# Optimization experiments

Hardware: AMD Instinct MI355X
Metric: run time of the kernel (lower is better)

## Reference

```python
import jax, jax.numpy as jnp
import numpy as np

N_NODES = 100000
IN_FEATS = 256
N_EDGES = 3200000
N_SEL = 4096
J_POOL = 50  # eval branch: inner loop over first 50 selected nodes


def setup_inputs() -> dict:
    key = jax.random.key(0)
    ks = jax.random.split(key, 16)
    x = jax.random.normal(ks[0], (N_NODES, IN_FEATS), dtype=jnp.float32)
    edge_index = jax.random.randint(ks[1], (2, N_EDGES), 0, N_NODES)
    nodes = jax.random.randint(ks[2], (N_SEL,), 0, N_NODES)
    s1 = 1.0 / np.sqrt(IN_FEATS)
    s2 = 1.0 / np.sqrt(32)
    s3 = 1.0 / np.sqrt(16)
    return {
        "x": x,
        "w1": jax.random.uniform(ks[3], (IN_FEATS, 32), jnp.float32, -s1, s1),
        "b1": jnp.zeros((32,), jnp.float32),
        "w2": jax.random.uniform(ks[4], (32, 16), jnp.float32, -s2, s2),
        "b2": jnp.zeros((16,), jnp.float32),
        "gate1_w": jax.random.normal(ks[5], (32, 4), jnp.float32) * 0.02,
        "e1_w": jax.random.uniform(ks[6], (4, 32, 16), jnp.float32, -s2, s2),
        "e1_b": jnp.zeros((4, 16), jnp.float32),
        "gate2_w": jax.random.normal(ks[7], (16, 4), jnp.float32) * 0.02,
        "e2_w": jax.random.uniform(ks[8], (4, 16, 2), jnp.float32, -s3, s3),
        "e2_b": jnp.zeros((4, 2), jnp.float32),
        "edge_index": edge_index,
        "nodes": nodes,
    }


def _gcn_conv(h, w, b, src, dst, n):
    hw = h @ w
    deg = jnp.zeros((n,), hw.dtype).at[dst].add(1.0)
    dis = jax.lax.rsqrt(jnp.maximum(deg, 1e-12))
    norm = dis[src] * dis[dst]
    msg = hw[src] * norm[:, None]
    return jax.ops.segment_sum(msg, dst, num_segments=n) + b


def _moe_top1(z, gate_w, ew, eb):
    # k=1 gating: softmax over a single selected logit == weight 1.0
    idx = jnp.argmax(z @ gate_w, axis=-1)              # [M]
    outs = jnp.einsum('mi,eio->meo', z, ew) + eb        # [M, E, O]
    return jnp.take_along_axis(outs, idx[:, None, None], axis=1)[:, 0]


def reference(x, w1, b1, w2, b2, gate1_w, e1_w, e1_b, gate2_w, e2_w, e2_b,
              edge_index, nodes):
    n = x.shape[0]
    loops = jnp.arange(n)
    src = jnp.concatenate([edge_index[0], loops])
    dst = jnp.concatenate([edge_index[1], loops])

    h = jax.nn.relu(_gcn_conv(x, w1, b1, src, dst, n))   # dropout: eval mode (identity)
    h = _gcn_conv(h, w2, b2, src, dst, n)                # [N, 16]

    # eval branch pairwise concat: i over all selected nodes, j over first 50
    hi = jnp.repeat(h[nodes], J_POOL, axis=0)            # [M, 16]
    hj = jnp.tile(h[nodes[:J_POOL]], (nodes.shape[0], 1))  # [M, 16]
    x_sim = jnp.concatenate([hi, hj], axis=-1)           # [M, 32]

    z = jax.nn.relu(_moe_top1(x_sim, gate1_w, e1_w, e1_b))
    z = _moe_top1(z, gate2_w, e2_w, e2_b)                # [M, 2]
    return jax.nn.log_softmax(z, axis=1), x_sim
```

## Files before the change

kernel.cpp:

```cpp
#include <hip/hip_runtime.h>
#include <hip/hip_fp16.h>
#include <math.h>


#define NPB 64
#define NB_PAD 2048
#define BATCH 8192
#define NSCAP 12288

typedef _Float16 half8 __attribute__((ext_vector_type(8)));
typedef float f32x4 __attribute__((ext_vector_type(4)));

__global__ void zero_kernel(int* __restrict__ p, int c) {
    int i = blockIdx.x * 256 + threadIdx.x;
    if (i < c) p[i] = 0;
}

__global__ __launch_bounds__(256) void histA_kernel(const int* __restrict__ ei,
                                                    int* __restrict__ bhist, int nE, int nb) {
    __shared__ int h[NB_PAD];
    int tid = threadIdx.x;
    for (int t = tid; t < nb; t += 256) h[t] = 0;
    __syncthreads();
    int base = blockIdx.x * 4096;
    for (int t = tid; t < 4096; t += 256) {
        int e = base + t;
        if (e < nE) atomicAdd(&h[ei[nE + e] >> 6], 1);
    }
    __syncthreads();
    for (int t = tid; t < nb; t += 256) { int c = h[t]; if (c) atomicAdd(&bhist[t], c); }
}

__global__ __launch_bounds__(256) void scanB_kernel(const int* __restrict__ bhist,
                                                    int* __restrict__ boffs,
                                                    int* __restrict__ gcur, int nb) {
    int t = threadIdx.x;
    int v[8], s = 0;
    #pragma unroll
    for (int i = 0; i < 8; ++i) { int c = t * 8 + i; v[i] = (c < nb) ? bhist[c] : 0; s += v[i]; }
    int lane = t & 63, wid = t >> 6;
    int incl = s;
    for (int d = 1; d < 64; d <<= 1) { int u = __shfl_up(incl, (unsigned)d, 64); if (lane >= d) incl += u; }
    __shared__ int ws[4];
    if (lane == 63) ws[wid] = incl;
    __syncthreads();
    int add = 0;
    for (int w = 0; w < wid; ++w) add += ws[w];
    incl += add;
    int excl = incl - s;
    #pragma unroll
    for (int i = 0; i < 8; ++i) {
        int c = t * 8 + i;
        if (c < nb) { boffs[c] = excl; gcur[c] = excl; }
        excl += v[i];
    }
    if (t == 0) boffs[nb] = ws[0] + ws[1] + ws[2] + ws[3];
}

__global__ __launch_bounds__(256) void scatterC_kernel(const int* __restrict__ ei,
                                                       int* __restrict__ gcur,
                                                       int* __restrict__ keys, int nE, int nb) {
    __shared__ int kbuf[BATCH];
    __shared__ unsigned short kbk[BATCH];
    __shared__ int lstart[NB_PAD];
    __shared__ int cursor[NB_PAD];
    __shared__ int gbase[NB_PAD];
    __shared__ int ws2[4];
    int tid = threadIdx.x;
    int base = blockIdx.x * BATCH;
    int cnt = nE - base; if (cnt > BATCH) cnt = BATCH;
    for (int t = tid; t < nb; t += 256) lstart[t] = 0;
    __syncthreads();
    for (int t = tid; t < cnt; t += 256)
        atomicAdd(&lstart[ei[nE + base + t] >> 6], 1);
    __syncthreads();
    {
        int v[8], s = 0;
        #pragma unroll
        for (int i = 0; i < 8; ++i) { int c = tid * 8 + i; v[i] = (c < nb) ? lstart[c] : 0; s += v[i]; }
        int lane = tid & 63, wid = tid >> 6;
        int incl = s;
        for (int d = 1; d < 64; d <<= 1) { int u = __shfl_up(incl, (unsigned)d, 64); if (lane >= d) incl += u; }
        if (lane == 63) ws2[wid] = incl;
        __syncthreads();
        int add = 0;
        for (int w = 0; w < wid; ++w) add += ws2[w];
        incl += add;
        int excl = incl - s;
        #pragma unroll
        for (int i = 0; i < 8; ++i) {
            int c = tid * 8 + i;
            if (c < nb) { lstart[c] = excl; cursor[c] = excl; }
            excl += v[i];
        }
    }
    __syncthreads();
    for (int t = tid; t < nb; t += 256) {
        int e = (t == nb - 1) ? cnt : lstart[t + 1];
        int c = e - lstart[t];
        gbase[t] = c ? atomicAdd(&gcur[t], c) : 0;
    }
    for (int t = tid; t < cnt; t += 256) {
        int d = ei[nE + base + t];
        int s = ei[base + t];
        int b = d >> 6;
        int pos = atomicAdd(&cursor[b], 1);
        kbuf[pos] = s | ((d & 63) << 17);
        kbk[pos] = (unsigned short)b;
    }
    __syncthreads();
    for (int j = tid; j < cnt; j += 256) {
        int b = kbk[j];
        keys[gbase[b] + (j - lstart[b])] = kbuf[j];
    }
}

__global__ __launch_bounds__(256) void nodesort_kernel(int* __restrict__ keys,
                                                       const int* __restrict__ boffs,
                                                       int* __restrict__ noffs,
                                                       float* __restrict__ dis,
                                                       int n, int nbuck) {
    __shared__ int kb[NSCAP];
    __shared__ int cnt[NPB], cur[NPB];
    int tid = threadIdx.x, b = blockIdx.x;
    int off = boffs[b], end = boffs[b + 1];
    int m = end - off; if (m > NSCAP) m = NSCAP;
    if (tid < NPB) cnt[tid] = 0;
    __syncthreads();
    for (int t = tid; t < m; t += 256) {
        int k = keys[off + t];
        kb[t] = k;
        atomicAdd(&cnt[k >> 17], 1);
    }
    __syncthreads();
    if (tid < NPB) {
        int v = cnt[tid];
        int incl = v;
        for (int d = 1; d < 64; d <<= 1) { int u = __shfl_up(incl, (unsigned)d, 64); if (tid >= d) incl += u; }
        int excl = incl - v;
        cur[tid] = excl;
        int node = b * NPB + tid;
        if (node < n) {
            noffs[node] = off + excl;
            dis[node] = rsqrtf((float)(v + 1));
        }
    }
    __syncthreads();
    for (int t = tid; t < m; t += 256) {
        int k = kb[t];
        int pos = atomicAdd(&cur[k >> 17], 1);
        keys[off + pos] = k & 0x1FFFF;
    }
    if (b == nbuck - 1 && tid == 0) noffs[n] = end;
}

__global__ __launch_bounds__(256) void hw1s_kernel(const float* __restrict__ x,
                                                   const float* __restrict__ w1,
                                                   const float* __restrict__ dis,
                                                   __half* __restrict__ hw1h, int n) {
    int tid = threadIdx.x;
    int lane = tid & 63;
    int wv = blockIdx.x * 4 + (tid >> 6);
    int nw = gridDim.x * 4;
    int mr = lane & 15, grp = lane >> 4;

    half8 bf0[8], bf1[8];
    #pragma unroll
    for (int kc = 0; kc < 8; ++kc) {
        half8 b0, b1v;
        #pragma unroll
        for (int e = 0; e < 8; ++e) {
            int k = kc * 32 + grp * 8 + e;
            b0[e]  = (_Float16)w1[k * 32 + mr];
            b1v[e] = (_Float16)w1[k * 32 + 16 + mr];
        }
        bf0[kc] = b0; bf1[kc] = b1v;
    }

    int nblk = (n + 15) >> 4;
    for (int blk = wv; blk < nblk; blk += nw) {
        int row = (blk << 4) + mr;
        int rowc = (row < n) ? row : n - 1;
        const float* xr = &x[(size_t)rowc * 256 + grp * 8];
        half8 af[8];
        #pragma unroll
        for (int kc = 0; kc < 8; ++kc) {
            float4 u = *(const float4*)&xr[kc * 32];
            float4 v = *(const float4*)&xr[kc * 32 + 4];
            half8 a;
            a[0] = (_Float16)u.x; a[1] = (_Float16)u.y;
            a[2] = (_Float16)u.z; a[3] = (_Float16)u.w;
            a[4] = (_Float16)v.x; a[5] = (_Float16)v.y;
            a[6] = (_Float16)v.z; a[7] = (_Float16)v.w;
            af[kc] = a;
        }
        f32x4 acc0 = {0.f, 0.f, 0.f, 0.f}, acc1 = {0.f, 0.f, 0.f, 0.f};
        #pragma unroll
        for (int kc = 0; kc < 8; ++kc)
            acc0 = __builtin_amdgcn_mfma_f32_16x16x32_f16(af[kc], bf0[kc], acc0, 0, 0, 0);
        #pragma unroll
        for (int kc = 0; kc < 8; ++kc)
            acc1 = __builtin_amdgcn_mfma_f32_16x16x32_f16(af[kc], bf1[kc], acc1, 0, 0, 0);
        #pragma unroll
        for (int i = 0; i < 4; ++i) {
            int orow = (blk << 4) + grp * 4 + i;
            if (orow < n) {
                float dn = dis[orow];
                hw1h[(size_t)orow * 32 + mr]      = __float2half(acc0[i] * dn);
                hw1h[(size_t)orow * 32 + 16 + mr] = __float2half(acc1[i] * dn);
            }
        }
    }
}

__global__ __launch_bounds__(256) void gatherG1_kernel(const __half* __restrict__ hw1h,
                                                       const float* __restrict__ dis,
                                                       const int* __restrict__ srcs,
                                                       const int* __restrict__ noffs,
                                                       const float* __restrict__ b1,
                                                       const float* __restrict__ w2,
                                                       float* __restrict__ hw2s, int n) {
    __shared__ float h1s[8][33];
    __shared__ float w2s[512];
    int tid = threadIdx.x;
    for (int t = tid; t < 512; t += 256) w2s[t] = w2[t];
    int g = tid >> 5, k = tid & 31;
    int node = blockIdx.x * 8 + g;
    float h = 0.f;
    if (node < n) {
        int off = noffs[node], end = noffs[node + 1];
        float acc = 0.f;
        int e = off;
        for (; e + 8 <= end; e += 8) {
            int s0 = srcs[e],     s1 = srcs[e + 1], s2 = srcs[e + 2], s3 = srcs[e + 3];
            int s4 = srcs[e + 4], s5 = srcs[e + 5], s6 = srcs[e + 6], s7 = srcs[e + 7];
            float v0 = __half2float(hw1h[(size_t)s0 * 32 + k]);
            float v1 = __half2float(hw1h[(size_t)s1 * 32 + k]);
            float v2 = __half2float(hw1h[(size_t)s2 * 32 + k]);
            float v3 = __half2float(hw1h[(size_t)s3 * 32 + k]);
            float v4 = __half2float(hw1h[(size_t)s4 * 32 + k]);
            float v5 = __half2float(hw1h[(size_t)s5 * 32 + k]);
            float v6 = __half2float(hw1h[(size_t)s6 * 32 + k]);
            float v7 = __half2float(hw1h[(size_t)s7 * 32 + k]);
            acc += ((v0 + v1) + (v2 + v3)) + ((v4 + v5) + (v6 + v7));
        }
        for (; e < end; ++e)
            acc += __half2float(hw1h[(size_t)srcs[e] * 32 + k]);
        float dn = dis[node];
        float self = __half2float(hw1h[(size_t)node * 32 + k]);
        h = fmaxf(dn * (acc + self) + b1[k], 0.f);
    }
    h1s[g][k] = h;
    __syncthreads();
    if (tid < 128) {
        int gg = tid >> 4, j = tid & 15;
        int nd = blockIdx.x * 8 + gg;
        if (nd < n) {
            float a = 0.f;
            #pragma unroll
            for (int c = 0; c < 32; ++c) a += h1s[gg][c] * w2s[c * 16 + j];
            hw2s[(size_t)nd * 16 + j] = a * dis[nd];
        }
    }
}

__global__ __launch_bounds__(256) void gatherG2_kernel(const float* __restrict__ hw2s,
                                                       const float* __restrict__ dis,
                                                       const int* __restrict__ srcs,
                                                       const int* __restrict__ noffs,
                                                       const int* __restrict__ nodes,
                                                       const float* __restrict__ b2,
                                                       float* __restrict__ h2, int nsel, int n) {
    int tid = threadIdx.x;
    int slot = tid >> 4, j = tid & 15;
    int i = blockIdx.x * 16 + slot;
    if (i >= nsel) return;
    int node = nodes[i];
    int off = noffs[node], end = noffs[node + 1];
    float acc = 0.f;
    int e = off;
    for (; e + 4 <= end; e += 4) {
        int s0 = srcs[e], s1 = srcs[e + 1], s2 = srcs[e + 2], s3 = srcs[e + 3];
        float v0 = hw2s[(size_t)s0 * 16 + j];
        float v1 = hw2s[(size_t)s1 * 16 + j];
        float v2 = hw2s[(size_t)s2 * 16 + j];
        float v3 = hw2s[(size_t)s3 * 16 + j];
        acc += (v0 + v1) + (v2 + v3);
    }
    for (; e < end; ++e) acc += hw2s[(size_t)srcs[e] * 16 + j];
    h2[(size_t)node * 16 + j] = dis[node] * (acc + hw2s[(size_t)node * 16 + j]) + b2[j];
}

__global__ __launch_bounds__(256) void pair_moe_kernel(const float* __restrict__ h2,
                                                       const int* __restrict__ nodes,
                                                       const float* __restrict__ gate1_w,
                                                       const float* __restrict__ e1_w,
                                                       const float* __restrict__ e1_b,
                                                       const float* __restrict__ gate2_w,
                                                       const float* __restrict__ e2_w,
                                                       const float* __restrict__ e2_b,
                                                       float* __restrict__ out1,
                                                       float* __restrict__ out2, int M) {
    __shared__ float hjs[50 * 16];
    __shared__ float g1s[32 * 4];
    __shared__ float e1ws[4 * 32 * 16];
    __shared__ float e1bs[4 * 16];
    __shared__ float g2s[16 * 4];
    __shared__ float e2ws[4 * 16 * 2];
    __shared__ float e2bs[4 * 2];
    int tid = threadIdx.x;
    for (int t = tid; t < 800; t += 256) { int j = t >> 4, c = t & 15; hjs[t] = h2[nodes[j] * 16 + c]; }
    for (int t = tid; t < 128; t += 256) g1s[t] = gate1_w[t];
    for (int t = tid; t < 2048; t += 256) e1ws[t] = e1_w[t];
    for (int t = tid; t < 64; t += 256) e1bs[t] = e1_b[t];
    for (int t = tid; t < 64; t += 256) g2s[t] = gate2_w[t];
    for (int t = tid; t < 128; t += 256) e2ws[t] = e2_w[t];
    if (tid < 8) e2bs[tid] = e2_b[tid];
    __syncthreads();

    int m = blockIdx.x * 256 + tid;
    if (m >= M) return;
    int i = m / 50, j = m - i * 50;

    float xs[32];
    int ni = nodes[i];
    float4 a0 = *(const float4*)&h2[ni * 16];
    float4 a1 = *(const float4*)&h2[ni * 16 + 4];
    float4 a2 = *(const float4*)&h2[ni * 16 + 8];
    float4 a3 = *(const float4*)&h2[ni * 16 + 12];
    xs[0]=a0.x; xs[1]=a0.y; xs[2]=a0.z; xs[3]=a0.w;
    xs[4]=a1.x; xs[5]=a1.y; xs[6]=a1.z; xs[7]=a1.w;
    xs[8]=a2.x; xs[9]=a2.y; xs[10]=a2.z; xs[11]=a2.w;
    xs[12]=a3.x; xs[13]=a3.y; xs[14]=a3.z; xs[15]=a3.w;
    #pragma unroll
    for (int c = 0; c < 16; ++c) xs[16 + c] = hjs[j * 16 + c];

    #pragma unroll
    for (int c = 0; c < 32; c += 4)
        *(float4*)&out2[(size_t)m * 32 + c] = make_float4(xs[c], xs[c+1], xs[c+2], xs[c+3]);

    float g[4] = {0.f, 0.f, 0.f, 0.f};
    #pragma unroll
    for (int c = 0; c < 32; ++c) {
        float xv = xs[c];
        #pragma unroll
        for (int e = 0; e < 4; ++e) g[e] += xv * g1s[c * 4 + e];
    }
    int idx = 0; float best = g[0];
    #pragma unroll
    for (int e = 1; e < 4; ++e) if (g[e] > best) { best = g[e]; idx = e; }
    float z[16];
    #pragma unroll
    for (int o = 0; o < 16; ++o) {
        float a = e1bs[idx * 16 + o];
        #pragma unroll
        for (int c = 0; c < 32; ++c) a += xs[c] * e1ws[(idx * 32 + c) * 16 + o];
        z[o] = fmaxf(a, 0.f);
    }

    float g2[4] = {0.f, 0.f, 0.f, 0.f};
    #pragma unroll
    for (int c = 0; c < 16; ++c) {
        float zv = z[c];
        #pragma unroll
        for (int e = 0; e < 4; ++e) g2[e] += zv * g2s[c * 4 + e];
    }
    int idx2 = 0; float best2 = g2[0];
    #pragma unroll
    for (int e = 1; e < 4; ++e) if (g2[e] > best2) { best2 = g2[e]; idx2 = e; }
    float z2[2];
    #pragma unroll
    for (int o = 0; o < 2; ++o) {
        float a = e2bs[idx2 * 2 + o];
        #pragma unroll
        for (int c = 0; c < 16; ++c) a += z[c] * e2ws[(idx2 * 16 + c) * 2 + o];
        z2[o] = a;
    }

    float mx = fmaxf(z2[0], z2[1]);
    float l = logf(expf(z2[0] - mx) + expf(z2[1] - mx));
    out1[(size_t)m * 2 + 0] = z2[0] - mx - l;
    out1[(size_t)m * 2 + 1] = z2[1] - mx - l;
}

extern "C" void kernel_launch(void* const* d_in, const int* in_sizes, int n_in,
                              void* d_out, int out_size, void* d_ws, size_t ws_size,
                              hipStream_t stream) {
    const float* x       = (const float*)d_in[0];
    const float* w1      = (const float*)d_in[1];
    const float* b1      = (const float*)d_in[2];
    const float* w2      = (const float*)d_in[3];
    const float* b2      = (const float*)d_in[4];
    const float* gate1_w = (const float*)d_in[5];
    const float* e1_w    = (const float*)d_in[6];
    const float* e1_b    = (const float*)d_in[7];
    const float* gate2_w = (const float*)d_in[8];
    const float* e2_w    = (const float*)d_in[9];
    const float* e2_b    = (const float*)d_in[10];
    const int*   ei      = (const int*)d_in[11];
    const int*   nodes   = (const int*)d_in[12];

    const int n    = in_sizes[0] / 256;
    const int nE   = in_sizes[11] / 2;
    const int nsel = in_sizes[12];
    const int M    = nsel * 50;
    const int nb   = (n + NPB - 1) / NPB;

    size_t off = 0;
    auto alloc = [&](size_t bytes) -> void* {
        void* p = (char*)d_ws + off;
        off += (bytes + 255) & ~(size_t)255;
        return p;
    };
    float*  dis    = (float*)alloc((size_t)n * 4);
    int*    bhist  = (int*)alloc((size_t)nb * 4);
    int*    boffs  = (int*)alloc((size_t)(nb + 1) * 4);
    int*    gcur   = (int*)alloc((size_t)nb * 4);
    int*    noffs  = (int*)alloc((size_t)(n + 1) * 4);
    int*    keys   = (int*)alloc((size_t)nE * 4);
    __half* hw1h   = (__half*)alloc((size_t)n * 32 * 2);
    float*  hw2s   = (float*)alloc((size_t)n * 16 * 4);
    float*  h2     = (float*)alloc((size_t)n * 16 * 4);
    if (off > ws_size) return;

    float* out1 = (float*)d_out;
    float* out2 = out1 + (size_t)M * 2;

    zero_kernel<<<(nb + 255) / 256, 256, 0, stream>>>(bhist, nb);
    histA_kernel<<<(nE + 4095) / 4096, 256, 0, stream>>>(ei, bhist, nE, nb);
    scanB_kernel<<<1, 256, 0, stream>>>(bhist, boffs, gcur, nb);
    scatterC_kernel<<<(nE + BATCH - 1) / BATCH, 256, 0, stream>>>(ei, gcur, keys, nE, nb);
    nodesort_kernel<<<nb, 256, 0, stream>>>(keys, boffs, noffs, dis, n, nb);
    hw1s_kernel<<<768, 256, 0, stream>>>(x, w1, dis, hw1h, n);
    gatherG1_kernel<<<(n + 7) / 8, 256, 0, stream>>>(hw1h, dis, keys, noffs, b1, w2, hw2s, n);
    gatherG2_kernel<<<(nsel + 15) / 16, 256, 0, stream>>>(hw2s, dis, keys, noffs, nodes, b2,
                                                          h2, nsel, n);
    pair_moe_kernel<<<(M + 255) / 256, 256, 0, stream>>>(h2, nodes, gate1_w, e1_w, e1_b,
                                                         gate2_w, e2_w, e2_b, out1, out2, M);
}
```

Before: 208.7 us.

## Split layer-1 features into two half tables and gather with half2 lanes

```diff
diff --git a/kernel.cpp b/kernel.cpp
--- a/kernel.cpp
+++ b/kernel.cpp
@@ -157,7 +157,8 @@
 __global__ __launch_bounds__(256) void hw1s_kernel(const float* __restrict__ x,
                                                    const float* __restrict__ w1,
                                                    const float* __restrict__ dis,
-                                                   __half* __restrict__ hw1h, int n) {
+                                                   __half* __restrict__ hw1hA,
+                                                   __half* __restrict__ hw1hB, int n) {
     int tid = threadIdx.x;
     int lane = tid & 63;
     int wv = blockIdx.x * 4 + (tid >> 6);
@@ -206,14 +207,15 @@
             int orow = (blk << 4) + grp * 4 + i;
             if (orow < n) {
                 float dn = dis[orow];
-                hw1h[(size_t)orow * 32 + mr]      = __float2half(acc0[i] * dn);
-                hw1h[(size_t)orow * 32 + 16 + mr] = __float2half(acc1[i] * dn);
+                hw1hA[(size_t)orow * 16 + mr] = __float2half(acc0[i] * dn);
+                hw1hB[(size_t)orow * 16 + mr] = __float2half(acc1[i] * dn);
             }
         }
     }
 }
 
-__global__ __launch_bounds__(256) void gatherG1_kernel(const __half* __restrict__ hw1h,
+__global__ __launch_bounds__(256) void gatherG1_kernel(const __half2* __restrict__ hw1hA2,
+                                                       const __half2* __restrict__ hw1hB2,
                                                        const float* __restrict__ dis,
                                                        const int* __restrict__ srcs,
                                                        const int* __restrict__ noffs,
@@ -224,33 +226,55 @@
     __shared__ float w2s[512];
     int tid = threadIdx.x;
     for (int t = tid; t < 512; t += 256) w2s[t] = w2[t];
-    int g = tid >> 5, k = tid & 31;
+    int g = tid >> 5, l = tid & 31;
+    int f2 = l & 7, eo = l >> 3;
     int node = blockIdx.x * 8 + g;
-    float h = 0.f;
     if (node < n) {
         int off = noffs[node], end = noffs[node + 1];
-        float acc = 0.f;
-        int e = off;
-        for (; e + 8 <= end; e += 8) {
-            int s0 = srcs[e],     s1 = srcs[e + 1], s2 = srcs[e + 2], s3 = srcs[e + 3];
-            int s4 = srcs[e + 4], s5 = srcs[e + 5], s6 = srcs[e + 6], s7 = srcs[e + 7];
-            float v0 = __half2float(hw1h[(size_t)s0 * 32 + k]);
-            float v1 = __half2float(hw1h[(size_t)s1 * 32 + k]);
-            float v2 = __half2float(hw1h[(size_t)s2 * 32 + k]);
-            float v3 = __half2float(hw1h[(size_t)s3 * 32 + k]);
-            float v4 = __half2float(hw1h[(size_t)s4 * 32 + k]);
-            float v5 = __half2float(hw1h[(size_t)s5 * 32 + k]);
-            float v6 = __half2float(hw1h[(size_t)s6 * 32 + k]);
-            float v7 = __half2float(hw1h[(size_t)s7 * 32 + k]);
-            acc += ((v0 + v1) + (v2 + v3)) + ((v4 + v5) + (v6 + v7));
-        }
-        for (; e < end; ++e)
-            acc += __half2float(hw1h[(size_t)srcs[e] * 32 + k]);
+        float ax = 0.f, ay = 0.f, bx = 0.f, by = 0.f;
+        int e = off + eo;
+        for (; e + 12 < end; e += 16) {
+            int s0 = srcs[e], s1 = srcs[e + 4], s2 = srcs[e + 8], s3 = srcs[e + 12];
+            float2 v0 = __half22float2(hw1hA2[(size_t)s0 * 8 + f2]);
+            float2 v1 = __half22float2(hw1hA2[(size_t)s1 * 8 + f2]);
+            float2 v2 = __half22float2(hw1hA2[(size_t)s2 * 8 + f2]);
+            float2 v3 = __half22float2(hw1hA2[(size_t)s3 * 8 + f2]);
+            ax += (v0.x + v1.x) + (v2.x + v3.x);
+            ay += (v0.y + v1.y) + (v2.y + v3.y);
+        }
+        for (; e < end; e += 4) {
+            float2 v = __half22float2(hw1hA2[(size_t)srcs[e] * 8 + f2]);
+            ax += v.x; ay += v.y;
+        }
+        e = off + eo;
+        for (; e + 12 < end; e += 16) {
+            int s0 = srcs[e], s1 = srcs[e + 4], s2 = srcs[e + 8], s3 = srcs[e + 12];
+            float2 v0 = __half22float2(hw1hB2[(size_t)s0 * 8 + f2]);
+            float2 v1 = __half22float2(hw1hB2[(size_t)s1 * 8 + f2]);
+            float2 v2 = __half22float2(hw1hB2[(size_t)s2 * 8 + f2]);
+            float2 v3 = __half22float2(hw1hB2[(size_t)s3 * 8 + f2]);
+            bx += (v0.x + v1.x) + (v2.x + v3.x);
+            by += (v0.y + v1.y) + (v2.y + v3.y);
+        }
+        for (; e < end; e += 4) {
+            float2 v = __half22float2(hw1hB2[(size_t)srcs[e] * 8 + f2]);
+            bx += v.x; by += v.y;
+        }
+        ax += __shfl_xor(ax, 8, 64);  ax += __shfl_xor(ax, 16, 64);
+        ay += __shfl_xor(ay, 8, 64);  ay += __shfl_xor(ay, 16, 64);
+        bx += __shfl_xor(bx, 8, 64);  bx += __shfl_xor(bx, 16, 64);
+        by += __shfl_xor(by, 8, 64);  by += __shfl_xor(by, 16, 64);
         float dn = dis[node];
-        float self = __half2float(hw1h[(size_t)node * 32 + k]);
-        h = fmaxf(dn * (acc + self) + b1[k], 0.f);
-    }
-    h1s[g][k] = h;
+        if (eo == 0) {
+            float2 sA = __half22float2(hw1hA2[(size_t)node * 8 + f2]);
+            h1s[g][2 * f2]     = fmaxf(dn * (ax + sA.x) + b1[2 * f2], 0.f);
+            h1s[g][2 * f2 + 1] = fmaxf(dn * (ay + sA.y) + b1[2 * f2 + 1], 0.f);
+        } else if (eo == 1) {
+            float2 sB = __half22float2(hw1hB2[(size_t)node * 8 + f2]);
+            h1s[g][16 + 2 * f2] = fmaxf(dn * (bx + sB.x) + b1[16 + 2 * f2], 0.f);
+            h1s[g][17 + 2 * f2] = fmaxf(dn * (by + sB.y) + b1[17 + 2 * f2], 0.f);
+        }
+    }
     __syncthreads();
     if (tid < 128) {
         int gg = tid >> 4, j = tid & 15;
@@ -418,7 +442,8 @@
     int*    gcur   = (int*)alloc((size_t)nb * 4);
     int*    noffs  = (int*)alloc((size_t)(n + 1) * 4);
     int*    keys   = (int*)alloc((size_t)nE * 4);
-    __half* hw1h   = (__half*)alloc((size_t)n * 32 * 2);
+    __half* hw1hA  = (__half*)alloc((size_t)n * 16 * 2);
+    __half* hw1hB  = (__half*)alloc((size_t)n * 16 * 2);
     float*  hw2s   = (float*)alloc((size_t)n * 16 * 4);
     float*  h2     = (float*)alloc((size_t)n * 16 * 4);
     if (off > ws_size) return;
@@ -431,8 +456,9 @@
     scanB_kernel<<<1, 256, 0, stream>>>(bhist, boffs, gcur, nb);
     scatterC_kernel<<<(nE + BATCH - 1) / BATCH, 256, 0, stream>>>(ei, gcur, keys, nE, nb);
     nodesort_kernel<<<nb, 256, 0, stream>>>(keys, boffs, noffs, dis, n, nb);
-    hw1s_kernel<<<768, 256, 0, stream>>>(x, w1, dis, hw1h, n);
-    gatherG1_kernel<<<(n + 7) / 8, 256, 0, stream>>>(hw1h, dis, keys, noffs, b1, w2, hw2s, n);
+    hw1s_kernel<<<768, 256, 0, stream>>>(x, w1, dis, hw1hA, hw1hB, n);
+    gatherG1_kernel<<<(n + 7) / 8, 256, 0, stream>>>((const __half2*)hw1hA, (const __half2*)hw1hB,
+                                                     dis, keys, noffs, b1, w2, hw2s, n);
     gatherG2_kernel<<<(nsel + 15) / 16, 256, 0, stream>>>(hw2s, dis, keys, noffs, nodes, b2,
                                                           h2, nsel, n);
     pair_moe_kernel<<<(M + 255) / 256, 256, 0, stream>>>(h2, nodes, gate1_w, e1_w, e1_b,
```

Measured after the change: 224.3 us. 1.07x slower.
